# Kernel optimization log

Hardware: AMD Instinct MI355X
Metric: run time of the kernel (lower is better)

## Reference

```python
import jax, jax.numpy as jnp
import numpy as np

N_NODES = 100000
N_EDGES = 1600000
HIDDEN = 128
N_LAYERS = 3
N_GRAPHS = 100
EPS = 1e-5


def setup_inputs() -> dict:
    key = jax.random.key(0)
    ks = jax.random.split(key, 9)
    node = jax.random.normal(ks[0], (N_NODES, HIDDEN), dtype=jnp.float32)
    edge_index = jax.random.randint(ks[1], (2, N_EDGES), 0, N_NODES, dtype=jnp.int32)
    edge_attr = jax.random.uniform(ks[2], (N_EDGES,), dtype=jnp.float32)
    batch_ptr = jnp.sort(jax.random.randint(ks[3], (N_NODES,), 0, N_GRAPHS, dtype=jnp.int32))
    W = jax.random.normal(ks[4], (N_LAYERS, HIDDEN, HIDDEN), dtype=jnp.float32) * (1.0 / np.sqrt(HIDDEN))
    b = jax.random.normal(ks[5], (N_LAYERS, HIDDEN), dtype=jnp.float32) * 0.02
    gn_weight = jnp.ones((N_LAYERS, HIDDEN), dtype=jnp.float32)
    gn_bias = jnp.zeros((N_LAYERS, HIDDEN), dtype=jnp.float32)
    gn_alpha = jnp.ones((N_LAYERS, HIDDEN), dtype=jnp.float32)
    return {"node": node, "edge_index": edge_index, "edge_attr": edge_attr,
            "batch_ptr": batch_ptr, "W": W, "b": b, "gn_weight": gn_weight,
            "gn_bias": gn_bias, "gn_alpha": gn_alpha}


def reference(node, edge_index, edge_attr, batch_ptr, W, b, gn_weight, gn_bias, gn_alpha):
    N, d = node.shape
    src, dst = edge_index[0], edge_index[1]
    # GCN normalization with self-loops (weight 1), as in PyG gcn_norm
    loop = jnp.arange(N, dtype=src.dtype)
    src_a = jnp.concatenate([src, loop])
    dst_a = jnp.concatenate([dst, loop])
    w_a = jnp.concatenate([edge_attr, jnp.ones((N,), dtype=edge_attr.dtype)])
    deg = jax.ops.segment_sum(w_a, dst_a, num_segments=N)
    dis = jnp.where(deg > 0, deg ** -0.5, 0.0)
    norm = dis[src_a] * w_a * dis[dst_a]  # [E+N]

    counts = jax.ops.segment_sum(jnp.ones((N,), node.dtype), batch_ptr,
                                 num_segments=N_GRAPHS)[:, None]  # [G,1]

    for l in range(W.shape[0]):
        # GCNConv: linear transform, then gather-normalize-scatter over edges
        h = node @ W[l]  # [N,d]
        agg = jax.ops.segment_sum(norm[:, None] * h[src_a], dst_a, num_segments=N) + b[l]
        # GraphNorm: per-graph mean shift (scaled by alpha) and variance norm
        mean = jax.ops.segment_sum(agg, batch_ptr, num_segments=N_GRAPHS) / counts  # [G,d]
        sub = agg - gn_alpha[l] * mean[batch_ptr]
        var = jax.ops.segment_sum(sub * sub, batch_ptr, num_segments=N_GRAPHS) / counts
        node = jax.nn.relu(gn_weight[l] * sub * jax.lax.rsqrt(var[batch_ptr] + EPS) + gn_bias[l])
    return node
```

## Files before the change

### kernel.cpp

```cpp
#include <hip/hip_runtime.h>
#include <cstdint>

#define N_N 100000
#define N_E 1600000
#define HID 128
#define N_G 100
#define EPSF 1e-5f

#define NB   256
#define EPB  ((N_E + NB - 1) / NB)
#define NBKT ((N_N + 255) >> 8)

static inline int ceil_div(int a, int b){ return (a + b - 1) / b; }

typedef __attribute__((ext_vector_type(8))) short bf16x8;
typedef __attribute__((ext_vector_type(4))) float f32x4;

__device__ inline unsigned short f2bf(float f){
  unsigned int u = __float_as_uint(f);
  unsigned int r = u + 0x7fffu + ((u >> 16) & 1u);
  return (unsigned short)(r >> 16);
}
__device__ inline void fma8(float* acc, float nv, uint4 u){
  acc[0] += nv * __uint_as_float(u.x << 16);
  acc[1] += nv * __uint_as_float(u.x & 0xffff0000u);
  acc[2] += nv * __uint_as_float(u.y << 16);
  acc[3] += nv * __uint_as_float(u.y & 0xffff0000u);
  acc[4] += nv * __uint_as_float(u.z << 16);
  acc[5] += nv * __uint_as_float(u.z & 0xffff0000u);
  acc[6] += nv * __uint_as_float(u.w << 16);
  acc[7] += nv * __uint_as_float(u.w & 0xffff0000u);
}

__global__ void k_wt3(const float* __restrict__ W, unsigned short* __restrict__ Wt,
                      int* __restrict__ gstart, int* __restrict__ gend){
  int i = blockIdx.x * 256 + threadIdx.x;
  if (i < N_G){ gstart[i] = 0; gend[i] = 0; }
  if (i >= 3 * HID * HID) return;
  int l = i >> 14;
  int r = i & 16383;
  int n = r >> 7, k = r & 127;
  Wt[i] = f2bf(W[l * HID * HID + k * HID + n]);
}

__global__ void k_bnd(const int* __restrict__ bp, int* __restrict__ gstart,
                      int* __restrict__ gend){
  int i = blockIdx.x * 256 + threadIdx.x;
  if (i >= N_N) return;
  int g = bp[i];
  if (i == 0 || bp[i - 1] != g) gstart[g] = i;
  if (i == N_N - 1 || bp[i + 1] != g) gend[g] = i + 1;
}

__global__ __launch_bounds__(256) void k_hist(const int* __restrict__ dst,
                                              int* __restrict__ counts){
  __shared__ int h[NBKT];
  int t = threadIdx.x, blk = blockIdx.x;
  for (int i = t; i < NBKT; i += 256) h[i] = 0;
  __syncthreads();
  int e0 = blk * EPB, e1 = min(e0 + EPB, N_E);
  for (int e = e0 + t; e < e1; e += 256)
    atomicAdd(&h[dst[e] >> 8], 1);
  __syncthreads();
  for (int i = t; i < NBKT; i += 256) counts[i * NB + blk] = h[i];
}

__global__ __launch_bounds__(256) void k_scanA(int* __restrict__ data,
                                               int* __restrict__ bsum, int n){
  __shared__ int s[256];
  int t = threadIdx.x;
  int i = blockIdx.x * 256 + t;
  int v = (i < n) ? data[i] : 0;
  s[t] = v; __syncthreads();
  #pragma unroll
  for (int off = 1; off < 256; off <<= 1){
    int tmp = (t >= off) ? s[t - off] : 0;
    __syncthreads();
    s[t] += tmp;
    __syncthreads();
  }
  if (i < n) data[i] = s[t] - v;
  if (t == 255) bsum[blockIdx.x] = s[255];
}

__global__ __launch_bounds__(512) void k_scanB(int* __restrict__ bsum, int nblocks){
  __shared__ int s[512];
  int t = threadIdx.x;
  int v = (t < nblocks) ? bsum[t] : 0;
  s[t] = v; __syncthreads();
  #pragma unroll
  for (int off = 1; off < 512; off <<= 1){
    int tmp = (t >= off) ? s[t - off] : 0;
    __syncthreads();
    s[t] += tmp;
    __syncthreads();
  }
  if (t < nblocks) bsum[t] = s[t] - v;
}

__global__ __launch_bounds__(256) void k_part(const int* __restrict__ src,
                                              const int* __restrict__ dst,
                                              const float* __restrict__ w,
                                              const int* __restrict__ coff,
                                              const int* __restrict__ bsum,
                                              int2* __restrict__ part){
  __shared__ int off[NBKT];
  int t = threadIdx.x, blk = blockIdx.x;
  for (int i = t; i < NBKT; i += 256)
    off[i] = coff[i * NB + blk] + bsum[i];
  __syncthreads();
  int e0 = blk * EPB, e1 = min(e0 + EPB, N_E);
  for (int e = e0 + t; e < e1; e += 256){
    int d = dst[e];
    int pos = atomicAdd(&off[d >> 8], 1);
    part[pos] = make_int2(src[e] | ((d & 255) << 24), __float_as_int(w[e]));
  }
}

__global__ __launch_bounds__(256) void k_csr(const int* __restrict__ coff,
                                             const int* __restrict__ bsum,
                                             const int2* __restrict__ part,
                                             int2* __restrict__ edge8,
                                             int* __restrict__ ptr,
                                             float* __restrict__ dis,
                                             float* __restrict__ nself){
  __shared__ int h[256];
  __shared__ int c[256];
  __shared__ float wsum[256];
  __shared__ int s[256];
  int t = threadIdx.x, b = blockIdx.x;
  int base  = coff[b * NB] + bsum[b];
  int base2 = (b + 1 < NBKT) ? coff[(b + 1) * NB] + bsum[b + 1] : N_E;
  h[t] = 0; c[t] = 0; wsum[t] = 0.f;
  __syncthreads();
  for (int e = base + t; e < base2; e += 256){
    int2 v = part[e];
    int local = ((unsigned int)v.x) >> 24;
    atomicAdd(&h[local], 1);
    atomicAdd(&wsum[local], __int_as_float(v.y));
  }
  __syncthreads();
  int v0 = h[t];
  s[t] = v0; __syncthreads();
  #pragma unroll
  for (int off = 1; off < 256; off <<= 1){
    int tmp = (t >= off) ? s[t - off] : 0;
    __syncthreads();
    s[t] += tmp;
    __syncthreads();
  }
  int mybase = base + s[t] - v0;
  int node = (b << 8) + t;
  float dv = rsqrtf(1.0f + wsum[t]);
  if (node < N_N){
    ptr[node] = mybase;
    dis[node] = dv;
    nself[node] = dv * dv;
  }
  if (b == NBKT - 1 && t == 0) ptr[N_N] = N_E;
  h[t] = mybase;
  __syncthreads();
  wsum[t] = dv;
  __syncthreads();
  for (int e = base + t; e < base2; e += 256){
    int2 v = part[e];
    int local = ((unsigned int)v.x) >> 24;
    int pos = h[local] + atomicAdd(&c[local], 1);
    edge8[pos] = make_int2(v.x & 0x00ffffff,
                           __float_as_int(__int_as_float(v.y) * wsum[local]));
  }
}

__global__ void k_ne(const float* __restrict__ dis, int2* __restrict__ edge8){
  int e = blockIdx.x * 256 + threadIdx.x;
  if (e >= N_E) return;
  int2 v = edge8[e];
  v.y = __float_as_int(__int_as_float(v.y) * dis[v.x]);
  edge8[e] = v;
}

__global__ __launch_bounds__(256) void k_gemm(const float* __restrict__ X,
                                              const float* __restrict__ agg,
                                              int fused,
                                              const int* __restrict__ bp,
                                              const float* __restrict__ mean,
                                              const float* __restrict__ rstd,
                                              const float* __restrict__ alpha,
                                              const float* __restrict__ gwv,
                                              const float* __restrict__ gbv,
                                              const unsigned short* __restrict__ Wt,
                                              unsigned short* __restrict__ Hb, int nrows){
  __shared__ unsigned short lA[64 * 136];
  __shared__ unsigned short lB[128 * 136];
  int tid = threadIdx.x;
  int row0 = blockIdx.x * 64;

  #pragma unroll
  for (int i = 0; i < 8; ++i){
    int c = tid + i * 256;
    int r = c >> 4, cc = c & 15;
    *(uint4*)&lB[r * 136 + cc * 8] = ((const uint4*)Wt)[c];
  }
  #pragma unroll
  for (int i = 0; i < 8; ++i){
    int c = tid + i * 256;
    int r = c >> 5, cc = c & 31;
    int gr = row0 + r;
    float4 v = make_float4(0.f, 0.f, 0.f, 0.f);
    if (gr < nrows){
      if (!fused){
        v = *(const float4*)(X + (size_t)gr * HID + cc * 4);
      } else {
        int g = bp[gr];
        float4 a  = *(const float4*)(agg  + (size_t)gr * HID + cc * 4);
        float4 m  = *(const float4*)(mean + g * HID + cc * 4);
        float4 rs = *(const float4*)(rstd + g * HID + cc * 4);
        float4 al = *(const float4*)(alpha + cc * 4);
        float4 wv = *(const float4*)(gwv + cc * 4);
        float4 bv = *(const float4*)(gbv + cc * 4);
        v.x = fmaxf(wv.x * (a.x - al.x * m.x) * rs.x + bv.x, 0.f);
        v.y = fmaxf(wv.y * (a.y - al.y * m.y) * rs.y + bv.y, 0.f);
        v.z = fmaxf(wv.z * (a.z - al.z * m.z) * rs.z + bv.z, 0.f);
        v.w = fmaxf(wv.w * (a.w - al.w * m.w) * rs.w + bv.w, 0.f);
      }
    }
    unsigned short pk[4] = {f2bf(v.x), f2bf(v.y), f2bf(v.z), f2bf(v.w)};
    *(uint2*)&lA[r * 136 + cc * 4] = *(const uint2*)pk;
  }
  __syncthreads();

  int wave = tid >> 6;
  int lane = tid & 63;
  int l16 = lane & 15;
  int quad = lane >> 4;
  int am = wave * 16 + l16;

  bf16x8 afr[4];
  #pragma unroll
  for (int kc = 0; kc < 4; ++kc)
    afr[kc] = *(const bf16x8*)&lA[am * 136 + kc * 32 + quad * 8];

  f32x4 accs[8];
  #pragma unroll
  for (int nt = 0; nt < 8; ++nt){
    f32x4 acc = {0.f, 0.f, 0.f, 0.f};
    int bn = nt * 16 + l16;
    #pragma unroll
    for (int kc = 0; kc < 4; ++kc){
      bf16x8 bfr = *(const bf16x8*)&lB[bn * 136 + kc * 32 + quad * 8];
      acc = __builtin_amdgcn_mfma_f32_16x16x32_bf16(afr[kc], bfr, acc, 0, 0, 0);
    }
    accs[nt] = acc;
  }

  __syncthreads();
  int crow = wave * 16 + quad * 4;
  #pragma unroll
  for (int nt = 0; nt < 8; ++nt){
    int col = nt * 16 + l16;
    #pragma unroll
    for (int r = 0; r < 4; ++r)
      lA[(crow + r) * 136 + col] = f2bf(accs[nt][r]);
  }
  __syncthreads();
  #pragma unroll
  for (int i = 0; i < 4; ++i){
    int idx = i * 256 + tid;
    int row = idx >> 4, c8 = idx & 15;
    int gr = row0 + row;
    if (gr < nrows)
      *(uint4*)&Hb[(size_t)gr * HID + c8 * 8] = *(const uint4*)&lA[row * 136 + c8 * 8];
  }
}

__global__ __launch_bounds__(256) void k_gather(const int* __restrict__ ptr,
                                                const int2* __restrict__ edge8,
                                                const unsigned short* __restrict__ Hb,
                                                const float* __restrict__ nself,
                                                const float* __restrict__ bias,
                                                float* __restrict__ agg){
  int t = blockIdx.x * 256 + threadIdx.x;
  int node = t >> 4;
  if (node >= N_N) return;
  int lane = t & 15;
  const uint4* h16 = (const uint4*)Hb;
  float ns = nself[node];
  uint4 hu = h16[(size_t)node * 16 + lane];
  float4 b0 = ((const float4*)bias)[lane * 2];
  float4 b1 = ((const float4*)bias)[lane * 2 + 1];
  float acc[8] = {b0.x, b0.y, b0.z, b0.w, b1.x, b1.y, b1.z, b1.w};
  fma8(acc, ns, hu);

  int e0 = ptr[node], e1 = ptr[node + 1];
  int e = e0;
  for (; e + 4 <= e1; e += 4){
    int2 ev0 = edge8[e + 0];
    int2 ev1 = edge8[e + 1];
    int2 ev2 = edge8[e + 2];
    int2 ev3 = edge8[e + 3];
    uint4 r0 = h16[(size_t)ev0.x * 16 + lane];
    uint4 r1 = h16[(size_t)ev1.x * 16 + lane];
    uint4 r2 = h16[(size_t)ev2.x * 16 + lane];
    uint4 r3 = h16[(size_t)ev3.x * 16 + lane];
    fma8(acc, __int_as_float(ev0.y), r0);
    fma8(acc, __int_as_float(ev1.y), r1);
    fma8(acc, __int_as_float(ev2.y), r2);
    fma8(acc, __int_as_float(ev3.y), r3);
  }
  for (; e < e1; ++e){
    int2 ev = edge8[e];
    uint4 r0 = h16[(size_t)ev.x * 16 + lane];
    fma8(acc, __int_as_float(ev.y), r0);
  }
  float4* ap = (float4*)(agg + (size_t)node * HID + lane * 8);
  ap[0] = make_float4(acc[0], acc[1], acc[2], acc[3]);
  ap[1] = make_float4(acc[4], acc[5], acc[6], acc[7]);
}

__global__ __launch_bounds__(256) void k_gstat(const float* __restrict__ agg,
                                               const int* __restrict__ gstart,
                                               const int* __restrict__ gend,
                                               float* __restrict__ psum,
                                               float* __restrict__ psq){
  __shared__ float ls[256], lq[256];
  int g = blockIdx.x >> 3, c = blockIdx.x & 7;
  int s = gstart[g], e = gend[g];
  int len = e - s;
  int r0 = s + ((len * c) >> 3);
  int r1 = s + ((len * (c + 1)) >> 3);
  int f = threadIdx.x & 127, rr = threadIdx.x >> 7;
  float sm = 0.f, sq = 0.f;
  for (int r = r0 + rr; r < r1; r += 2){
    float v = agg[(size_t)r * HID + f];
    sm += v; sq += v * v;
  }
  ls[threadIdx.x] = sm; lq[threadIdx.x] = sq;
  __syncthreads();
  if (rr == 0){
    psum[(size_t)blockIdx.x * HID + f] = ls[f] + ls[f + 128];
    psq [(size_t)blockIdx.x * HID + f] = lq[f] + lq[f + 128];
  }
}

__global__ void k_finstat(const float* __restrict__ psum, const float* __restrict__ psq,
                          const int* __restrict__ gstart, const int* __restrict__ gend,
                          const float* __restrict__ alpha,
                          float* __restrict__ mean, float* __restrict__ rstd){
  int i = blockIdx.x * 256 + threadIdx.x;
  if (i >= N_G * HID) return;
  int g = i >> 7, f = i & (HID - 1);
  float c = (float)(gend[g] - gstart[g]);
  float inv = c > 0.f ? 1.0f / c : 0.f;
  float sm = 0.f, sq = 0.f;
  #pragma unroll
  for (int k = 0; k < 8; ++k){
    sm += psum[(size_t)(g * 8 + k) * HID + f];
    sq += psq [(size_t)(g * 8 + k) * HID + f];
  }
  float m = sm * inv;
  float ex2 = sq * inv;
  float al = alpha[f];
  float var = ex2 - m * m * al * (2.0f - al);
  mean[i] = m;
  rstd[i] = rsqrtf(var + EPSF);
}

__global__ void k_out(const float* __restrict__ agg, const int* __restrict__ bp,
                      const float* __restrict__ mean, const float* __restrict__ rstd,
                      const float* __restrict__ alpha, const float* __restrict__ gw,
                      const float* __restrict__ gb, float* __restrict__ out){
  int idx = blockIdx.x * 256 + threadIdx.x;
  if (idx >= N_N * 32) return;
  int i = idx >> 5, q = idx & 31;
  int g = bp[i];
  float4 a  = ((const float4*)agg)[idx];
  float4 m  = ((const float4*)mean)[g * 32 + q];
  float4 r  = ((const float4*)rstd)[g * 32 + q];
  float4 al = ((const float4*)alpha)[q];
  float4 wv = ((const float4*)gw)[q];
  float4 bv = ((const float4*)gb)[q];
  float4 o;
  o.x = fmaxf(wv.x * (a.x - al.x * m.x) * r.x + bv.x, 0.f);
  o.y = fmaxf(wv.y * (a.y - al.y * m.y) * r.y + bv.y, 0.f);
  o.z = fmaxf(wv.z * (a.z - al.z * m.z) * r.z + bv.z, 0.f);
  o.w = fmaxf(wv.w * (a.w - al.w * m.w) * r.w + bv.w, 0.f);
  ((float4*)out)[idx] = o;
}


extern "C" void kernel_launch(void* const* d_in, const int* in_sizes, int n_in,
                              void* d_out, int out_size, void* d_ws, size_t ws_size,
                              hipStream_t stream){
  const float* node0 = (const float*)d_in[0];
  const int*   eidx  = (const int*)d_in[1];
  const float* eattr = (const float*)d_in[2];
  const int*   bp    = (const int*)d_in[3];
  const float* W     = (const float*)d_in[4];
  const float* bias  = (const float*)d_in[5];
  const float* gw    = (const float*)d_in[6];
  const float* gb    = (const float*)d_in[7];
  const float* ga    = (const float*)d_in[8];
  float* out = (float*)d_out;
  const int* src = eidx;
  const int* dst = eidx + N_E;

  char* p = (char*)d_ws;
  auto carve = [&](size_t nbytes) -> char* {
    char* q = p; p += (nbytes + 255) & ~(size_t)255; return q;
  };
  float* dis    = (float*)carve((size_t)N_N * 4);
  float* nself  = (float*)carve((size_t)N_N * 4);
  int*   gstart = (int*)  carve((size_t)N_G * 4);
  int*   gend   = (int*)  carve((size_t)N_G * 4);
  int*   coff   = (int*)  carve((size_t)NBKT * NB * 4);
  int*   bsum   = (int*)  carve((size_t)512 * 4);
  int*   ptr    = (int*)  carve((size_t)(N_N + 1) * 4);
  int2*  edge8  = (int2*) carve((size_t)N_E * 8);
  unsigned short* hb = (unsigned short*)carve((size_t)N_N * HID * 2);
  unsigned short* wt = (unsigned short*)carve((size_t)3 * HID * HID * 2);
  float* agg    = (float*)carve((size_t)N_N * HID * 4);
  float* mean   = (float*)carve((size_t)N_G * HID * 4);
  float* rstd   = (float*)carve((size_t)N_G * HID * 4);
  float* psum   = (float*)carve((size_t)N_G * 8 * HID * 4);
  float* psq    = (float*)carve((size_t)N_G * 8 * HID * 4);
  int2*  part   = (int2*)agg;

  int nscan = NBKT * NB;
  int nscan_blocks = ceil_div(nscan, 256);

  k_wt3  <<<ceil_div(3 * HID * HID, 256), 256, 0, stream>>>(W, wt, gstart, gend);
  k_bnd  <<<ceil_div(N_N, 256), 256, 0, stream>>>(bp, gstart, gend);
  k_hist <<<NB, 256, 0, stream>>>(dst, coff);
  k_scanA<<<nscan_blocks, 256, 0, stream>>>(coff, bsum, nscan);
  k_scanB<<<1, 512, 0, stream>>>(bsum, nscan_blocks);
  k_part <<<NB, 256, 0, stream>>>(src, dst, eattr, coff, bsum, part);
  k_csr  <<<NBKT, 256, 0, stream>>>(coff, bsum, part, edge8, ptr, dis, nself);
  k_ne   <<<ceil_div(N_E, 256), 256, 0, stream>>>(dis, edge8);

  for (int l = 0; l < 3; ++l){
    if (l == 0){
      k_gemm <<<ceil_div(N_N, 64), 256, 0, stream>>>(node0, nullptr, 0,
                 nullptr, nullptr, nullptr, nullptr, nullptr, nullptr,
                 wt, hb, N_N);
    } else {
      k_gemm <<<ceil_div(N_N, 64), 256, 0, stream>>>(nullptr, agg, 1,
                 bp, mean, rstd, ga + (l - 1) * HID, gw + (l - 1) * HID,
                 gb + (l - 1) * HID, wt + (size_t)l * HID * HID, hb, N_N);
    }
    k_gather <<<ceil_div(N_N * 16, 256), 256, 0, stream>>>(ptr, edge8, hb, nself,
                 bias + l * HID, agg);
    k_gstat  <<<N_G * 8, 256, 0, stream>>>(agg, gstart, gend, psum, psq);
    k_finstat<<<ceil_div(N_G * HID, 256), 256, 0, stream>>>(psum, psq, gstart, gend,
                 ga + l * HID, mean, rstd);
  }
  k_out <<<ceil_div(N_N * 32, 256), 256, 0, stream>>>(agg, bp, mean, rstd,
             ga + 2 * HID, gw + 2 * HID, gb + 2 * HID, out);
}
```

Before: 562.4 us.

## Fuse per-graph GraphNorm statistics into gather kernel via graph-aligned row chunks

The gather kernel now assigns each block a 16-row chunk that stays inside one graph, using a prefix table of chunk counts per graph built once by a new single-thread kernel. Each block reduces sum and sum-of-squares of its aggregated rows in shared memory and writes per-chunk partials, so the separate stats kernel and its re-read of the fp32 agg buffer are gone. Finstat then sums a variable number of chunk partials per graph. The cost is a binary search per block, some idle rows at graph edges, and a larger partials buffer with longer serial loops in finstat.

```diff
diff --git a/kernel.cpp b/kernel.cpp
--- a/kernel.cpp
+++ b/kernel.cpp
@@ -10,6 +10,8 @@
 #define NB   256
 #define EPB  ((N_E + NB - 1) / NB)
 #define NBKT ((N_N + 255) >> 8)
+
+#define MAXCH (N_N / 16 + N_G)
 
 static inline int ceil_div(int a, int b){ return (a + b - 1) / b; }
 
@@ -50,6 +52,19 @@
   int g = bp[i];
   if (i == 0 || bp[i - 1] != g) gstart[g] = i;
   if (i == N_N - 1 || bp[i + 1] != g) gend[g] = i + 1;
+}
+
+__global__ void k_cbase(const int* __restrict__ gstart, const int* __restrict__ gend,
+                        int* __restrict__ cbase){
+  if (threadIdx.x == 0){
+    int run = 0;
+    for (int g = 0; g < N_G; ++g){
+      cbase[g] = run;
+      int len = gend[g] - gstart[g];
+      run += (len + 15) >> 4;
+    }
+    cbase[N_G] = run;
+  }
 }
 
 __global__ __launch_bounds__(256) void k_hist(const int* __restrict__ dst,
@@ -278,84 +293,90 @@
                                                 const unsigned short* __restrict__ Hb,
                                                 const float* __restrict__ nself,
                                                 const float* __restrict__ bias,
-                                                float* __restrict__ agg){
-  int t = blockIdx.x * 256 + threadIdx.x;
-  int node = t >> 4;
-  if (node >= N_N) return;
-  int lane = t & 15;
+                                                float* __restrict__ agg,
+                                                const int* __restrict__ cbase,
+                                                const int* __restrict__ gstart,
+                                                const int* __restrict__ gend,
+                                                float* __restrict__ psum,
+                                                float* __restrict__ psq){
+  __shared__ float rs[16][132];
+  __shared__ float rq[16][132];
+  int blk = blockIdx.x;
+  if (blk >= cbase[N_G]) return;
+  int lo = 0, hi = N_G;
+  while (hi - lo > 1){ int mid = (lo + hi) >> 1; if (cbase[mid] <= blk) lo = mid; else hi = mid; }
+  int g = lo;
+  int row0 = gstart[g] + (blk - cbase[g]) * 16;
+  int rend = gend[g];
+  int trow = threadIdx.x >> 4;
+  int lane = threadIdx.x & 15;
+  int node = row0 + trow;
+  bool active = node < rend;
   const uint4* h16 = (const uint4*)Hb;
-  float ns = nself[node];
-  uint4 hu = h16[(size_t)node * 16 + lane];
   float4 b0 = ((const float4*)bias)[lane * 2];
   float4 b1 = ((const float4*)bias)[lane * 2 + 1];
   float acc[8] = {b0.x, b0.y, b0.z, b0.w, b1.x, b1.y, b1.z, b1.w};
-  fma8(acc, ns, hu);
-
-  int e0 = ptr[node], e1 = ptr[node + 1];
-  int e = e0;
-  for (; e + 4 <= e1; e += 4){
-    int2 ev0 = edge8[e + 0];
-    int2 ev1 = edge8[e + 1];
-    int2 ev2 = edge8[e + 2];
-    int2 ev3 = edge8[e + 3];
-    uint4 r0 = h16[(size_t)ev0.x * 16 + lane];
-    uint4 r1 = h16[(size_t)ev1.x * 16 + lane];
-    uint4 r2 = h16[(size_t)ev2.x * 16 + lane];
-    uint4 r3 = h16[(size_t)ev3.x * 16 + lane];
-    fma8(acc, __int_as_float(ev0.y), r0);
-    fma8(acc, __int_as_float(ev1.y), r1);
-    fma8(acc, __int_as_float(ev2.y), r2);
-    fma8(acc, __int_as_float(ev3.y), r3);
-  }
-  for (; e < e1; ++e){
-    int2 ev = edge8[e];
-    uint4 r0 = h16[(size_t)ev.x * 16 + lane];
-    fma8(acc, __int_as_float(ev.y), r0);
-  }
-  float4* ap = (float4*)(agg + (size_t)node * HID + lane * 8);
-  ap[0] = make_float4(acc[0], acc[1], acc[2], acc[3]);
-  ap[1] = make_float4(acc[4], acc[5], acc[6], acc[7]);
-}
-
-__global__ __launch_bounds__(256) void k_gstat(const float* __restrict__ agg,
-                                               const int* __restrict__ gstart,
-                                               const int* __restrict__ gend,
-                                               float* __restrict__ psum,
-                                               float* __restrict__ psq){
-  __shared__ float ls[256], lq[256];
-  int g = blockIdx.x >> 3, c = blockIdx.x & 7;
-  int s = gstart[g], e = gend[g];
-  int len = e - s;
-  int r0 = s + ((len * c) >> 3);
-  int r1 = s + ((len * (c + 1)) >> 3);
-  int f = threadIdx.x & 127, rr = threadIdx.x >> 7;
-  float sm = 0.f, sq = 0.f;
-  for (int r = r0 + rr; r < r1; r += 2){
-    float v = agg[(size_t)r * HID + f];
-    sm += v; sq += v * v;
-  }
-  ls[threadIdx.x] = sm; lq[threadIdx.x] = sq;
-  __syncthreads();
-  if (rr == 0){
-    psum[(size_t)blockIdx.x * HID + f] = ls[f] + ls[f + 128];
-    psq [(size_t)blockIdx.x * HID + f] = lq[f] + lq[f + 128];
+  if (active){
+    float ns = nself[node];
+    uint4 hu = h16[(size_t)node * 16 + lane];
+    fma8(acc, ns, hu);
+    int e0 = ptr[node], e1 = ptr[node + 1];
+    int e = e0;
+    for (; e + 4 <= e1; e += 4){
+      int2 ev0 = edge8[e + 0];
+      int2 ev1 = edge8[e + 1];
+      int2 ev2 = edge8[e + 2];
+      int2 ev3 = edge8[e + 3];
+      uint4 r0 = h16[(size_t)ev0.x * 16 + lane];
+      uint4 r1 = h16[(size_t)ev1.x * 16 + lane];
+      uint4 r2 = h16[(size_t)ev2.x * 16 + lane];
+      uint4 r3 = h16[(size_t)ev3.x * 16 + lane];
+      fma8(acc, __int_as_float(ev0.y), r0);
+      fma8(acc, __int_as_float(ev1.y), r1);
+      fma8(acc, __int_as_float(ev2.y), r2);
+      fma8(acc, __int_as_float(ev3.y), r3);
+    }
+    for (; e < e1; ++e){
+      int2 ev = edge8[e];
+      uint4 r0 = h16[(size_t)ev.x * 16 + lane];
+      fma8(acc, __int_as_float(ev.y), r0);
+    }
+    float4* ap = (float4*)(agg + (size_t)node * HID + lane * 8);
+    ap[0] = make_float4(acc[0], acc[1], acc[2], acc[3]);
+    ap[1] = make_float4(acc[4], acc[5], acc[6], acc[7]);
+  }
+  int f = lane * 8;
+  #pragma unroll
+  for (int j = 0; j < 8; ++j){
+    float v = active ? acc[j] : 0.f;
+    rs[trow][f + j] = v;
+    rq[trow][f + j] = v * v;
+  }
+  __syncthreads();
+  if (threadIdx.x < 128){
+    float s = 0.f, q = 0.f;
+    #pragma unroll
+    for (int r = 0; r < 16; ++r){ s += rs[r][threadIdx.x]; q += rq[r][threadIdx.x]; }
+    psum[(size_t)blk * HID + threadIdx.x] = s;
+    psq [(size_t)blk * HID + threadIdx.x] = q;
   }
 }
 
 __global__ void k_finstat(const float* __restrict__ psum, const float* __restrict__ psq,
+                          const int* __restrict__ cbase,
                           const int* __restrict__ gstart, const int* __restrict__ gend,
                           const float* __restrict__ alpha,
                           float* __restrict__ mean, float* __restrict__ rstd){
   int i = blockIdx.x * 256 + threadIdx.x;
   if (i >= N_G * HID) return;
   int g = i >> 7, f = i & (HID - 1);
+  int c0 = cbase[g], c1 = cbase[g + 1];
   float c = (float)(gend[g] - gstart[g]);
   float inv = c > 0.f ? 1.0f / c : 0.f;
   float sm = 0.f, sq = 0.f;
-  #pragma unroll
-  for (int k = 0; k < 8; ++k){
-    sm += psum[(size_t)(g * 8 + k) * HID + f];
-    sq += psq [(size_t)(g * 8 + k) * HID + f];
+  for (int k = c0; k < c1; ++k){
+    sm += psum[(size_t)k * HID + f];
+    sq += psq [(size_t)k * HID + f];
   }
   float m = sm * inv;
   float ex2 = sq * inv;
@@ -412,6 +433,7 @@
   float* nself  = (float*)carve((size_t)N_N * 4);
   int*   gstart = (int*)  carve((size_t)N_G * 4);
   int*   gend   = (int*)  carve((size_t)N_G * 4);
+  int*   cbase  = (int*)  carve((size_t)(N_G + 1) * 4);
   int*   coff   = (int*)  carve((size_t)NBKT * NB * 4);
   int*   bsum   = (int*)  carve((size_t)512 * 4);
   int*   ptr    = (int*)  carve((size_t)(N_N + 1) * 4);
@@ -421,8 +443,8 @@
   float* agg    = (float*)carve((size_t)N_N * HID * 4);
   float* mean   = (float*)carve((size_t)N_G * HID * 4);
   float* rstd   = (float*)carve((size_t)N_G * HID * 4);
-  float* psum   = (float*)carve((size_t)N_G * 8 * HID * 4);
-  float* psq    = (float*)carve((size_t)N_G * 8 * HID * 4);
+  float* psum   = (float*)carve((size_t)MAXCH * HID * 4);
+  float* psq    = (float*)carve((size_t)MAXCH * HID * 4);
   int2*  part   = (int2*)agg;
 
   int nscan = NBKT * NB;
@@ -430,6 +452,7 @@
 
   k_wt3  <<<ceil_div(3 * HID * HID, 256), 256, 0, stream>>>(W, wt, gstart, gend);
   k_bnd  <<<ceil_div(N_N, 256), 256, 0, stream>>>(bp, gstart, gend);
+  k_cbase<<<1, 64, 0, stream>>>(gstart, gend, cbase);
   k_hist <<<NB, 256, 0, stream>>>(dst, coff);
   k_scanA<<<nscan_blocks, 256, 0, stream>>>(coff, bsum, nscan);
   k_scanB<<<1, 512, 0, stream>>>(bsum, nscan_blocks);
@@ -447,11 +470,10 @@
                  bp, mean, rstd, ga + (l - 1) * HID, gw + (l - 1) * HID,
                  gb + (l - 1) * HID, wt + (size_t)l * HID * HID, hb, N_N);
     }
-    k_gather <<<ceil_div(N_N * 16, 256), 256, 0, stream>>>(ptr, edge8, hb, nself,
-                 bias + l * HID, agg);
-    k_gstat  <<<N_G * 8, 256, 0, stream>>>(agg, gstart, gend, psum, psq);
-    k_finstat<<<ceil_div(N_G * HID, 256), 256, 0, stream>>>(psum, psq, gstart, gend,
-                 ga + l * HID, mean, rstd);
+    k_gather <<<MAXCH, 256, 0, stream>>>(ptr, edge8, hb, nself,
+                 bias + l * HID, agg, cbase, gstart, gend, psum, psq);
+    k_finstat<<<ceil_div(N_G * HID, 256), 256, 0, stream>>>(psum, psq, cbase,
+                 gstart, gend, ga + l * HID, mean, rstd);
   }
   k_out <<<ceil_div(N_N * 32, 256), 256, 0, stream>>>(agg, bp, mean, rstd,
              ga + 2 * HID, gw + 2 * HID, gb + 2 * HID, out);
```

Result: slower. 574.6 us (+2.2%).

## Fold source-side degree scaling into GEMM epilogue and merge setup kernels

Applied to the files above, without the earlier changes.

The per-edge source normalization pass (k_ne) is removed. Instead the GEMM epilogue scales each output row by dis[row], so gathered features already carry the source factor and the self-loop weight becomes dis[node] rather than dis^2. The three setup kernels (weight transpose, graph bounds, edge histogram) are merged into one launch, with graph bounds now filled gap-aware so no separate zeroing is needed. This drops a full read-modify-write over the edge array and two launches. The cost is an extra dis load per row in each GEMM, and the per-row scale is applied before bf16 rounding, which slightly changes numerics.

```diff
diff --git a/kernel.cpp b/kernel.cpp
--- a/kernel.cpp
+++ b/kernel.cpp
@@ -10,6 +10,8 @@
 #define NB   256
 #define EPB  ((N_E + NB - 1) / NB)
 #define NBKT ((N_N + 255) >> 8)
+#define NBB  ((N_N + 255) / 256)
+#define NWT  ((3 * HID * HID) / 256)
 
 static inline int ceil_div(int a, int b){ return (a + b - 1) / b; }
 
@@ -32,37 +34,48 @@
   acc[7] += nv * __uint_as_float(u.w & 0xffff0000u);
 }
 
-__global__ void k_wt3(const float* __restrict__ W, unsigned short* __restrict__ Wt,
-                      int* __restrict__ gstart, int* __restrict__ gend){
-  int i = blockIdx.x * 256 + threadIdx.x;
-  if (i < N_G){ gstart[i] = 0; gend[i] = 0; }
-  if (i >= 3 * HID * HID) return;
-  int l = i >> 14;
-  int r = i & 16383;
-  int n = r >> 7, k = r & 127;
-  Wt[i] = f2bf(W[l * HID * HID + k * HID + n]);
-}
-
-__global__ void k_bnd(const int* __restrict__ bp, int* __restrict__ gstart,
-                      int* __restrict__ gend){
-  int i = blockIdx.x * 256 + threadIdx.x;
-  if (i >= N_N) return;
-  int g = bp[i];
-  if (i == 0 || bp[i - 1] != g) gstart[g] = i;
-  if (i == N_N - 1 || bp[i + 1] != g) gend[g] = i + 1;
-}
-
-__global__ __launch_bounds__(256) void k_hist(const int* __restrict__ dst,
-                                              int* __restrict__ counts){
-  __shared__ int h[NBKT];
+__global__ __launch_bounds__(256) void k_pre(const int* __restrict__ dst,
+                                             int* __restrict__ counts,
+                                             const int* __restrict__ bp,
+                                             int* __restrict__ gstart,
+                                             int* __restrict__ gend,
+                                             const float* __restrict__ W,
+                                             unsigned short* __restrict__ Wt){
   int t = threadIdx.x, blk = blockIdx.x;
-  for (int i = t; i < NBKT; i += 256) h[i] = 0;
-  __syncthreads();
-  int e0 = blk * EPB, e1 = min(e0 + EPB, N_E);
-  for (int e = e0 + t; e < e1; e += 256)
-    atomicAdd(&h[dst[e] >> 8], 1);
-  __syncthreads();
-  for (int i = t; i < NBKT; i += 256) counts[i * NB + blk] = h[i];
+  if (blk < NB){
+    __shared__ int h[NBKT];
+    for (int i = t; i < NBKT; i += 256) h[i] = 0;
+    __syncthreads();
+    int e0 = blk * EPB, e1 = min(e0 + EPB, N_E);
+    for (int e = e0 + t; e < e1; e += 256)
+      atomicAdd(&h[dst[e] >> 8], 1);
+    __syncthreads();
+    for (int i = t; i < NBKT; i += 256) counts[i * NB + blk] = h[i];
+  } else if (blk < NB + NBB){
+    int i = (blk - NB) * 256 + t;
+    if (i >= N_N) return;
+    int g = bp[i];
+    if (i == 0){
+      gstart[g] = 0;
+      for (int gg = 0; gg < g; ++gg){ gstart[gg] = 0; gend[gg] = 0; }
+    } else {
+      int pg = bp[i - 1];
+      if (pg != g){
+        gend[pg] = i; gstart[g] = i;
+        for (int gg = pg + 1; gg < g; ++gg){ gstart[gg] = i; gend[gg] = i; }
+      }
+    }
+    if (i == N_N - 1){
+      gend[g] = N_N;
+      for (int gg = g + 1; gg < N_G; ++gg){ gstart[gg] = N_N; gend[gg] = N_N; }
+    }
+  } else {
+    int j = (blk - NB - NBB) * 256 + t;
+    int l = j >> 14;
+    int r = j & 16383;
+    int n = r >> 7, k = r & 127;
+    Wt[j] = f2bf(W[l * HID * HID + k * HID + n]);
+  }
 }
 
 __global__ __launch_bounds__(256) void k_scanA(int* __restrict__ data,
@@ -122,8 +135,7 @@
                                              const int2* __restrict__ part,
                                              int2* __restrict__ edge8,
                                              int* __restrict__ ptr,
-                                             float* __restrict__ dis,
-                                             float* __restrict__ nself){
+                                             float* __restrict__ dis){
   __shared__ int h[256];
   __shared__ int c[256];
   __shared__ float wsum[256];
@@ -155,7 +167,6 @@
   if (node < N_N){
     ptr[node] = mybase;
     dis[node] = dv;
-    nself[node] = dv * dv;
   }
   if (b == NBKT - 1 && t == 0) ptr[N_N] = N_E;
   h[t] = mybase;
@@ -169,14 +180,6 @@
     edge8[pos] = make_int2(v.x & 0x00ffffff,
                            __float_as_int(__int_as_float(v.y) * wsum[local]));
   }
-}
-
-__global__ void k_ne(const float* __restrict__ dis, int2* __restrict__ edge8){
-  int e = blockIdx.x * 256 + threadIdx.x;
-  if (e >= N_E) return;
-  int2 v = edge8[e];
-  v.y = __float_as_int(__int_as_float(v.y) * dis[v.x]);
-  edge8[e] = v;
 }
 
 __global__ __launch_bounds__(256) void k_gemm(const float* __restrict__ X,
@@ -189,6 +192,7 @@
                                               const float* __restrict__ gwv,
                                               const float* __restrict__ gbv,
                                               const unsigned short* __restrict__ Wt,
+                                              const float* __restrict__ dis,
                                               unsigned short* __restrict__ Hb, int nrows){
   __shared__ unsigned short lA[64 * 136];
   __shared__ unsigned short lB[128 * 136];
@@ -253,14 +257,21 @@
     accs[nt] = acc;
   }
 
-  __syncthreads();
   int crow = wave * 16 + quad * 4;
+  float ds[4];
+  #pragma unroll
+  for (int r = 0; r < 4; ++r){
+    int grr = row0 + crow + r;
+    ds[r] = (grr < nrows) ? dis[grr] : 0.f;
+  }
+
+  __syncthreads();
   #pragma unroll
   for (int nt = 0; nt < 8; ++nt){
     int col = nt * 16 + l16;
     #pragma unroll
     for (int r = 0; r < 4; ++r)
-      lA[(crow + r) * 136 + col] = f2bf(accs[nt][r]);
+      lA[(crow + r) * 136 + col] = f2bf(accs[nt][r] * ds[r]);
   }
   __syncthreads();
   #pragma unroll
@@ -276,7 +287,7 @@
 __global__ __launch_bounds__(256) void k_gather(const int* __restrict__ ptr,
                                                 const int2* __restrict__ edge8,
                                                 const unsigned short* __restrict__ Hb,
-                                                const float* __restrict__ nself,
+                                                const float* __restrict__ dis,
                                                 const float* __restrict__ bias,
                                                 float* __restrict__ agg){
   int t = blockIdx.x * 256 + threadIdx.x;
@@ -284,7 +295,7 @@
   if (node >= N_N) return;
   int lane = t & 15;
   const uint4* h16 = (const uint4*)Hb;
-  float ns = nself[node];
+  float ns = dis[node];
   uint4 hu = h16[(size_t)node * 16 + lane];
   float4 b0 = ((const float4*)bias)[lane * 2];
   float4 b1 = ((const float4*)bias)[lane * 2 + 1];
@@ -409,7 +420,6 @@
     char* q = p; p += (nbytes + 255) & ~(size_t)255; return q;
   };
   float* dis    = (float*)carve((size_t)N_N * 4);
-  float* nself  = (float*)carve((size_t)N_N * 4);
   int*   gstart = (int*)  carve((size_t)N_G * 4);
   int*   gend   = (int*)  carve((size_t)N_G * 4);
   int*   coff   = (int*)  carve((size_t)NBKT * NB * 4);
@@ -428,26 +438,23 @@
   int nscan = NBKT * NB;
   int nscan_blocks = ceil_div(nscan, 256);
 
-  k_wt3  <<<ceil_div(3 * HID * HID, 256), 256, 0, stream>>>(W, wt, gstart, gend);
-  k_bnd  <<<ceil_div(N_N, 256), 256, 0, stream>>>(bp, gstart, gend);
-  k_hist <<<NB, 256, 0, stream>>>(dst, coff);
+  k_pre  <<<NB + NBB + NWT, 256, 0, stream>>>(dst, coff, bp, gstart, gend, W, wt);
   k_scanA<<<nscan_blocks, 256, 0, stream>>>(coff, bsum, nscan);
   k_scanB<<<1, 512, 0, stream>>>(bsum, nscan_blocks);
   k_part <<<NB, 256, 0, stream>>>(src, dst, eattr, coff, bsum, part);
-  k_csr  <<<NBKT, 256, 0, stream>>>(coff, bsum, part, edge8, ptr, dis, nself);
-  k_ne   <<<ceil_div(N_E, 256), 256, 0, stream>>>(dis, edge8);
+  k_csr  <<<NBKT, 256, 0, stream>>>(coff, bsum, part, edge8, ptr, dis);
 
   for (int l = 0; l < 3; ++l){
     if (l == 0){
       k_gemm <<<ceil_div(N_N, 64), 256, 0, stream>>>(node0, nullptr, 0,
                  nullptr, nullptr, nullptr, nullptr, nullptr, nullptr,
-                 wt, hb, N_N);
+                 wt, dis, hb, N_N);
     } else {
       k_gemm <<<ceil_div(N_N, 64), 256, 0, stream>>>(nullptr, agg, 1,
                  bp, mean, rstd, ga + (l - 1) * HID, gw + (l - 1) * HID,
-                 gb + (l - 1) * HID, wt + (size_t)l * HID * HID, hb, N_N);
+                 gb + (l - 1) * HID, wt + (size_t)l * HID * HID, dis, hb, N_N);
     }
-    k_gather <<<ceil_div(N_N * 16, 256), 256, 0, stream>>>(ptr, edge8, hb, nself,
+    k_gather <<<ceil_div(N_N * 16, 256), 256, 0, stream>>>(ptr, edge8, hb, dis,
                  bias + l * HID, agg);
     k_gstat  <<<N_G * 8, 256, 0, stream>>>(agg, gstart, gend, psum, psq);
     k_finstat<<<ceil_div(N_G * HID, 256), 256, 0, stream>>>(psum, psq, gstart, gend,
```

Measured after the change: 544.4 us. -3.2%, faster.
